# Performance work log

Hardware: AMD Instinct MI355X
Metric: run time of the kernel (lower is better)

## Reference

```python
import jax, jax.numpy as jnp
import numpy as np

B, S, D = 8, 1024, 2048
H, HD = 16, 128          # n_heads, head_dim (H*HD == D)
ROPE = 64                # rotary dims per head (front slice)
MAXB, MAXS = 10, 1024    # kv-cache buffer sizes (hardcoded in module)
START_POS = 0


def _apply_rope(x, cos_half, sin_half):
    # x: (BH, S, ROPE); cos/sin_half: (S, ROPE//2) -> tiled to (S, ROPE)
    cos_full = jnp.concatenate([cos_half, cos_half], axis=-1)
    sin_full = jnp.concatenate([sin_half, sin_half], axis=-1)
    half = x.shape[-1] // 2
    x1, x2 = x[..., :half], x[..., half:]
    rotated = jnp.concatenate([-x2, x1], axis=-1)
    return x * cos_full + rotated * sin_full


def setup_inputs() -> dict:
    key = jax.random.key(0)
    ks = jax.random.split(key, 6)
    sc = 0.02
    x = jax.random.normal(ks[0], (B, S, D), dtype=jnp.float32)
    wq = jax.random.normal(ks[1], (D, D), dtype=jnp.float32) * sc
    wk = jax.random.normal(ks[2], (D, D), dtype=jnp.float32) * sc
    wv = jax.random.normal(ks[3], (D, D), dtype=jnp.float32) * sc
    wo = jax.random.normal(ks[4], (D, D), dtype=jnp.float32) * sc
    bq = jnp.zeros((D,), jnp.float32)
    bk = jnp.zeros((D,), jnp.float32)
    bv = jnp.zeros((D,), jnp.float32)
    bo = jnp.zeros((D,), jnp.float32)
    # RoPE tables (HF "half" layout): angles over positions
    half = ROPE // 2
    inv_freq = 1.0 / (10000.0 ** (jnp.arange(half, dtype=jnp.float32) / half))
    ang = jnp.arange(S, dtype=jnp.float32)[:, None] * inv_freq[None, :]  # (S, half)
    cos_half = jnp.cos(ang)
    sin_half = jnp.sin(ang)
    mask = jnp.zeros((S, S), jnp.float32)  # additive mask, (seq, end_pos)
    cache_k = jnp.zeros((MAXB, MAXS, H * HD), jnp.float32)
    cache_v = jnp.zeros((MAXB, MAXS, H * HD), jnp.float32)
    return {
        "x": x, "wq": wq, "bq": bq, "wk": wk, "bk": bk, "wv": wv, "bv": bv,
        "wo": wo, "bo": bo, "cos_half": cos_half, "sin_half": sin_half,
        "mask": mask, "cache_k": cache_k, "cache_v": cache_v,
        "start_pos": START_POS,
    }


def reference(x, wq, bq, wk, bk, wv, bv, wo, bo, cos_half, sin_half, mask,
              cache_k, cache_v, start_pos):
    b, s, _ = x.shape
    end_pos = start_pos + s
    # QKV projections (torch Linear: y = x @ W.T + b)
    q = (x @ wq.T + bq).reshape(b, s, H, HD)
    k = (x @ wk.T + bk).reshape(b, s, H, HD)
    v = (x @ wv.T + bv).reshape(b, s, H, HD)
    # Partial RoPE on the first ROPE dims of each head
    q_head = q[..., :ROPE].transpose(0, 2, 1, 3).reshape(b * H, s, ROPE)
    k_head = k[..., :ROPE].transpose(0, 2, 1, 3).reshape(b * H, s, ROPE)
    q_head = _apply_rope(q_head, cos_half, sin_half)
    k_head = _apply_rope(k_head, cos_half, sin_half)
    q_head = q_head.reshape(b, H, s, ROPE).transpose(0, 2, 1, 3)
    k_head = k_head.reshape(b, H, s, ROPE).transpose(0, 2, 1, 3)
    q = jnp.concatenate([q_head, q[..., ROPE:]], axis=-1)
    k = jnp.concatenate([k_head, k[..., ROPE:]], axis=-1)
    # KV-cache write then read (start_pos is a static python int)
    cache_k = jax.lax.dynamic_update_slice(cache_k, k.reshape(b, s, H * HD), (0, start_pos, 0))
    cache_v = jax.lax.dynamic_update_slice(cache_v, v.reshape(b, s, H * HD), (0, start_pos, 0))
    k_cached = cache_k[:b, :end_pos].reshape(b, end_pos, H, HD)
    v_cached = cache_v[:b, :end_pos].reshape(b, end_pos, H, HD)
    # Unnormalized attention: no softmax, no scaling
    scores = jnp.einsum('bshd,bthd->bsht', q, k_cached)  # (B,S,H,T)
    scores = scores + mask[:, None, :]                   # (S,1,T) broadcast
    a_sum = jnp.einsum('bsht,bthd->bshd', scores, v_cached)
    out = a_sum.reshape(b, s, H * HD) @ wo.T + bo
    return out
```

## Files before the change

kernel.cpp:

```cpp
#include <hip/hip_runtime.h>
#include <stdint.h>

#define B_ 8
#define S_ 1024
#define D_ 2048
#define H_ 16
#define HD_ 128
#define NROW 8192
#define NQKV 6144

typedef __bf16 bf16;
typedef bf16  bf16x8 __attribute__((ext_vector_type(8)));
typedef bf16  bf16x4 __attribute__((ext_vector_type(4)));
typedef float f32x4  __attribute__((ext_vector_type(4)));

#define AS1 __attribute__((address_space(1)))
#define AS3 __attribute__((address_space(3)))

__device__ __forceinline__ void gl_lds16(const bf16* g, bf16* l) {
  __builtin_amdgcn_global_load_lds((AS1 void*)g, (AS3 void*)l, 16, 0, 0);
}

__global__ __launch_bounds__(256) void prep(const float* __restrict__ x,
                                            const float* __restrict__ wq,
                                            const float* __restrict__ wk,
                                            const float* __restrict__ wv,
                                            const float* __restrict__ wo,
                                            const float* __restrict__ mask,
                                            const float* __restrict__ bq,
                                            const float* __restrict__ bk,
                                            const float* __restrict__ bv,
                                            bf16* __restrict__ xb,
                                            bf16* __restrict__ wqkvb,
                                            bf16* __restrict__ wob,
                                            bf16* __restrict__ maskb,
                                            float* __restrict__ bqkv) {
  long i = (long)blockIdx.x * 256 + threadIdx.x;
  if (i < 8650752) {
    const float* src; bf16* dst; long j;
    if (i < 4194304)      { src = x;    dst = xb;              j = i; }
    else if (i < 5242880) { src = wq;   dst = wqkvb;           j = i - 4194304; }
    else if (i < 6291456) { src = wk;   dst = wqkvb + 4194304; j = i - 5242880; }
    else if (i < 7340032) { src = wv;   dst = wqkvb + 8388608; j = i - 6291456; }
    else if (i < 8388608) { src = wo;   dst = wob;             j = i - 7340032; }
    else                  { src = mask; dst = maskb;           j = i - 8388608; }
    float4 v = reinterpret_cast<const float4*>(src)[j];
    bf16x4 o;
    o.x = (bf16)v.x; o.y = (bf16)v.y; o.z = (bf16)v.z; o.w = (bf16)v.w;
    reinterpret_cast<bf16x4*>(dst)[j] = o;
  } else {
    long e = (i - 8650752) * 4;
    const float* s = (e < 2048) ? bq + e : (e < 4096 ? bk + (e - 2048) : bv + (e - 4096));
    *reinterpret_cast<float4*>(bqkv + e) = *reinterpret_cast<const float4*>(s);
  }
}

#define READ_A4(QA, KS, Ab)                                                   \
  _Pragma("unroll") for (int mi = 0; mi < 4; mi++)                            \
    af[mi] = *reinterpret_cast<const bf16x8*>(                                \
        (Ab) + aoff + ((((QA)*4 + mi)*2) + (KS))*512);

#define READ_B4(KS, Bb)                                                       \
  _Pragma("unroll") for (int ni = 0; ni < 4; ni++)                            \
    bfr[ni] = *reinterpret_cast<const bf16x8*>(                               \
        (Bb) + boff + ((ni*2) + (KS))*512);

#define MFMA16(QA)                                                            \
  _Pragma("unroll") for (int mi = 0; mi < 4; mi++)                            \
  _Pragma("unroll") for (int ni = 0; ni < 4; ni++)                            \
    acc[(QA)*4 + mi][ni] = __builtin_amdgcn_mfma_f32_16x16x32_bf16(           \
        af[mi], bfr[ni], acc[(QA)*4 + mi][ni], 0, 0, 0);

#define STAGE_H0(An, Bn, koff)                                                \
  gl_lds16(agA + (koff),           (An) + wid*1024);                          \
  gl_lds16(agA + 128*la + (koff),  (An) + (wid + 8)*1024);                    \
  gl_lds16(agB + (koff),           (Bn) + wid*1024);                          \
  gl_lds16(agB + 128*lb + (koff),  (Bn) + (wid + 8)*1024);

#define STAGE_H1(An, Bn, koff)                                                \
  gl_lds16(agA + (koff) + 32,          (An) + wid*1024 + 512);                \
  gl_lds16(agA + 128*la + (koff) + 32, (An) + (wid + 8)*1024 + 512);          \
  gl_lds16(agB + (koff) + 32,          (Bn) + wid*1024 + 512);                \
  gl_lds16(agB + 128*lb + (koff) + 32, (Bn) + (wid + 8)*1024 + 512);

template <typename CT, bool BIAS, bool ACCUM>
__global__ __launch_bounds__(512, 2) void gemm256(const bf16* __restrict__ A,
                                                  const bf16* __restrict__ Bm,
                                                  const float* __restrict__ bias,
                                                  CT* __restrict__ C,
                                                  int M, int N, int K,
                                                  long la, long lb, long lc,
                                                  long za, long zb, long zc) {
  extern __shared__ __align__(16) bf16 lds[];
  const int z = blockIdx.z;
  A  += (long)z * za;
  Bm += (long)z * zb;
  C  += (long)z * zc;
  const int tid  = threadIdx.x;
  const int wid  = tid >> 6;
  const int lane = tid & 63;
  const int wm0 = (wid >> 2) * 128;
  const int wn0 = (wid & 3) * 64;
  const int m0 = blockIdx.y * 256, n0 = blockIdx.x * 256;

  const int rr = lane >> 2;
  const int cc = ((lane & 3) * 8) ^ ((rr & 8) << 1);
  const bf16* agA = A  + (long)(m0 + wid * 16 + rr) * la + cc;
  const bf16* agB = Bm + (long)(n0 + wid * 16 + rr) * lb + cc;

  const int swz  = ((lane >> 4) * 8) ^ ((lane & 8) << 1);
  const int aoff = (wm0 >> 4) * 1024 + (lane & 15) * 32 + swz;
  const int boff = (wn0 >> 4) * 1024 + (lane & 15) * 32 + swz;

  f32x4 acc[8][4] = {};
  const int NT = K >> 6;

  { bf16* An = lds; bf16* Bn = lds + 16384;
    STAGE_H0(An, Bn, 0); STAGE_H1(An, Bn, 0); }
  { bf16* An = lds + 32768; bf16* Bn = lds + 49152;
    STAGE_H0(An, Bn, 64); }

  for (int t = 0; t < NT; ++t) {
    const bf16* Ab = lds + (t & 1) * 32768;
    const bf16* Bb = Ab + 16384;
    bf16* An1 = lds + ((t & 1) ^ 1) * 32768;
    bf16* Bn1 = An1 + 16384;
    bf16* An2 = lds + (t & 1) * 32768;
    bf16* Bn2 = An2 + 16384;
    const bool pf1 = (t + 1) < NT;
    const bool pf2 = (t + 2) < NT;
    bf16x8 af[4], bfr[4];

    if (pf1) asm volatile("s_waitcnt vmcnt(8)" ::: "memory");
    else     asm volatile("s_waitcnt vmcnt(4)" ::: "memory");
    __builtin_amdgcn_s_barrier();
    READ_A4(0, 0, Ab); READ_B4(0, Bb);
    if (pf1) { STAGE_H1(An1, Bn1, (long)(t + 1) * 64); }
    asm volatile("s_waitcnt lgkmcnt(0)" ::: "memory");
    __builtin_amdgcn_sched_barrier(0);
    __builtin_amdgcn_s_setprio(1); MFMA16(0); __builtin_amdgcn_s_setprio(0);

    READ_A4(1, 0, Ab);
    asm volatile("s_waitcnt lgkmcnt(0)" ::: "memory");
    __builtin_amdgcn_sched_barrier(0);
    __builtin_amdgcn_s_setprio(1); MFMA16(1); __builtin_amdgcn_s_setprio(0);

    if (pf1) asm volatile("s_waitcnt vmcnt(8)" ::: "memory");
    else     asm volatile("s_waitcnt vmcnt(0)" ::: "memory");
    __builtin_amdgcn_s_barrier();
    READ_A4(0, 1, Ab); READ_B4(1, Bb);
    if (pf2) { STAGE_H0(An2, Bn2, (long)(t + 2) * 64); }
    asm volatile("s_waitcnt lgkmcnt(0)" ::: "memory");
    __builtin_amdgcn_sched_barrier(0);
    __builtin_amdgcn_s_setprio(1); MFMA16(0); __builtin_amdgcn_s_setprio(0);

    READ_A4(1, 1, Ab);
    asm volatile("s_waitcnt lgkmcnt(0)" ::: "memory");
    __builtin_amdgcn_sched_barrier(0);
    __builtin_amdgcn_s_setprio(1); MFMA16(1); __builtin_amdgcn_s_setprio(0);
  }

#pragma unroll
  for (int mi = 0; mi < 8; mi++) {
#pragma unroll
    for (int ni = 0; ni < 4; ni++) {
      const int col = n0 + wn0 + ni * 16 + (lane & 15);
      float bv = 0.0f;
      if constexpr (BIAS) bv = bias[col];
      const long base = (long)(m0 + wm0 + mi * 16 + (lane >> 4) * 4) * lc + col;
#pragma unroll
      for (int r = 0; r < 4; r++) {
        float v = acc[mi][ni][r] + bv;
        if constexpr (ACCUM) v += (float)C[base + (long)r * lc];
        C[base + (long)r * lc] = (CT)v;
      }
    }
  }
}

template <typename CT, bool BIAS, bool ACCUM>
__global__ __launch_bounds__(256) void gemm_bt(const bf16* __restrict__ A,
                                               const bf16* __restrict__ Bm,
                                               const float* __restrict__ bias,
                                               CT* __restrict__ C,
                                               int M, int N, int K,
                                               long la, long lb, long lc,
                                               long za, long zb, long zc) {
  __shared__ __align__(16) bf16 As[128 * 32];
  __shared__ __align__(16) bf16 Bs[128 * 32];
  const int z = blockIdx.z;
  A  += (long)z * za;
  Bm += (long)z * zb;
  C  += (long)z * zc;
  const int tid = threadIdx.x;
  const int w = tid >> 6, l = tid & 63;
  const int wm = (w & 1) * 64, wn = (w >> 1) * 64;
  const int m0 = blockIdx.y * 128, n0 = blockIdx.x * 128;
  const int lr = l & 15, lk = (l >> 4) * 8;
  const int er = (l >> 4) * 4;

  const bf16* ag = A  + (long)(m0 + (tid >> 2)) * la + (tid & 3) * 8;
  const bf16* bg = Bm + (long)(n0 + (tid >> 2)) * lb + (tid & 3) * 8;
  bf16* al = As + (w * 16) * 32;
  bf16* bl = Bs + (w * 16) * 32;

  f32x4 acc[4][4] = {};

  for (int k0 = 0; k0 < K; k0 += 32) {
    gl_lds16(ag + k0,            al);
    gl_lds16(ag + 64 * la + k0,  al + 64 * 32);
    gl_lds16(bg + k0,            bl);
    gl_lds16(bg + 64 * lb + k0,  bl + 64 * 32);
    __syncthreads();
    bf16x8 afr[4], bfr[4];
#pragma unroll
    for (int mi = 0; mi < 4; mi++)
      afr[mi] = *reinterpret_cast<const bf16x8*>(As + (wm + mi * 16 + lr) * 32 + lk);
#pragma unroll
    for (int ni = 0; ni < 4; ni++)
      bfr[ni] = *reinterpret_cast<const bf16x8*>(Bs + (wn + ni * 16 + lr) * 32 + lk);
#pragma unroll
    for (int mi = 0; mi < 4; mi++)
#pragma unroll
      for (int ni = 0; ni < 4; ni++)
        acc[mi][ni] = __builtin_amdgcn_mfma_f32_16x16x32_bf16(afr[mi], bfr[ni], acc[mi][ni], 0, 0, 0);
    __syncthreads();
  }

#pragma unroll
  for (int mi = 0; mi < 4; mi++) {
#pragma unroll
    for (int ni = 0; ni < 4; ni++) {
      const int col = n0 + wn + ni * 16 + lr;
      float bv = 0.0f;
      if constexpr (BIAS) bv = bias[col];
      const long base = (long)(m0 + wm + mi * 16 + er) * lc + col;
#pragma unroll
      for (int r = 0; r < 4; r++) {
        float v = acc[mi][ni][r] + bv;
        if constexpr (ACCUM) v += (float)C[base + (long)r * lc];
        C[base + (long)r * lc] = (CT)v;
      }
    }
  }
}

__global__ __launch_bounds__(256) void rope_qk(bf16* __restrict__ QKV,
                                               const float* __restrict__ ch,
                                               const float* __restrict__ sh) {
  int idx = blockIdx.x * 256 + threadIdx.x;
  if (idx >= NROW * H_ * 2 * 32) return;
  int hd = idx & 31;
  int qk = (idx >> 5) & 1;
  int h  = (idx >> 6) & 15;
  int row = idx >> 10;
  int s = row & (S_ - 1);
  long base = (long)row * NQKV + qk * 2048 + h * HD_ + hd;
  float a  = (float)QKV[base];
  float b2 = (float)QKV[base + 32];
  float c = ch[s * 32 + hd], sn = sh[s * 32 + hd];
  QKV[base]      = (bf16)(a * c - b2 * sn);
  QKV[base + 32] = (bf16)(b2 * c + a * sn);
}

__global__ __launch_bounds__(256) void kvtrans(const bf16* __restrict__ QKV,
                                               bf16* __restrict__ Kt,
                                               bf16* __restrict__ Vt) {
  __shared__ unsigned short T[128 * 130];
  const int bid = blockIdx.x;
  const int tb = bid & 7, bh = (bid >> 3) & 127, kv = bid >> 10;
  const int b = bh >> 4, h = bh & 15;
  const int tid = threadIdx.x;
  const bf16* src = QKV + (long)(b * S_ + tb * 128) * NQKV + 2048 + kv * 2048 + h * HD_;
#pragma unroll
  for (int it = 0; it < 8; it++) {
    int chunk = it * 256 + tid;
    int r = chunk >> 4, hc = (chunk & 15) * 8;
    bf16x8 v = *reinterpret_cast<const bf16x8*>(src + (long)r * NQKV + hc);
    union { bf16x8 v8; unsigned short u[8]; } u8; u8.v8 = v;
#pragma unroll
    for (int j = 0; j < 8; j++) T[r * 130 + hc + j] = u8.u[j];
  }
  __syncthreads();
  bf16* dst = (kv ? Vt : Kt) + (long)bh * HD_ * S_ + tb * 128;
#pragma unroll
  for (int it = 0; it < 8; it++) {
    int chunk = it * 256 + tid;
    int hd = chunk >> 4, tc = (chunk & 15) * 8;
    union { bf16x8 v8; unsigned short u[8]; } u8;
#pragma unroll
    for (int j = 0; j < 8; j++) u8.u[j] = T[(tc + j) * 130 + hd];
    *reinterpret_cast<bf16x8*>(dst + (long)hd * S_ + tc) = u8.v8;
  }
}

__global__ __launch_bounds__(256) void qw2_gemm(const bf16* __restrict__ QKV,
                                                const bf16* __restrict__ W2,
                                                bf16* __restrict__ Ob) {
  __shared__ __align__(16) bf16 As[128 * 32];
  __shared__ __align__(16) bf16 Bs[128 * 32];
  const int z = blockIdx.z;
  const int b = z >> 4, h = z & 15;
  const int m0 = blockIdx.y * 128;
  const int tid = threadIdx.x;
  const int w = tid >> 6, l = tid & 63;
  const int wm = (w & 1) * 64, wn = (w >> 1) * 64;
  const int lr = l & 15, lk = (l >> 4) * 8;
  const int er = (l >> 4) * 4;

  const bf16* ag = QKV + (long)(b * S_ + m0 + (tid >> 2)) * NQKV + h * HD_ + (tid & 3) * 8;
  const bf16* bg = W2 + (long)z * (HD_ * HD_) + (tid >> 2) * HD_ + (tid & 3) * 8;
  bf16* al = As + (w * 16) * 32;
  bf16* bl = Bs + (w * 16) * 32;

  f32x4 acc[4][4] = {};

#pragma unroll
  for (int k0 = 0; k0 < HD_; k0 += 32) {
    gl_lds16(ag + k0,                   al);
    gl_lds16(ag + (long)64 * NQKV + k0, al + 64 * 32);
    gl_lds16(bg + k0,                   bl);
    gl_lds16(bg + 64 * HD_ + k0,        bl + 64 * 32);
    __syncthreads();
    bf16x8 afr[4], bfr[4];
#pragma unroll
    for (int mi = 0; mi < 4; mi++)
      afr[mi] = *reinterpret_cast<const bf16x8*>(As + (wm + mi * 16 + lr) * 32 + lk);
#pragma unroll
    for (int ni = 0; ni < 4; ni++)
      bfr[ni] = *reinterpret_cast<const bf16x8*>(Bs + (wn + ni * 16 + lr) * 32 + lk);
#pragma unroll
    for (int mi = 0; mi < 4; mi++)
#pragma unroll
      for (int ni = 0; ni < 4; ni++)
        acc[mi][ni] = __builtin_amdgcn_mfma_f32_16x16x32_bf16(afr[mi], bfr[ni], acc[mi][ni], 0, 0, 0);
    __syncthreads();
  }

#pragma unroll
  for (int mi = 0; mi < 4; mi++) {
#pragma unroll
    for (int ni = 0; ni < 4; ni++) {
      const int col = h * HD_ + wn + ni * 16 + lr;
#pragma unroll
      for (int r = 0; r < 4; r++) {
        const int sl = m0 + wm + mi * 16 + er + r;
        const long idx = (long)(b * S_ + sl) * D_ + col;
        Ob[idx] = (bf16)((float)Ob[idx] + acc[mi][ni][r]);
      }
    }
  }
}

extern "C" void kernel_launch(void* const* d_in, const int* in_sizes, int n_in,
                              void* d_out, int out_size, void* d_ws, size_t ws_size,
                              hipStream_t stream) {
  const float* x   = (const float*)d_in[0];
  const float* wq  = (const float*)d_in[1];
  const float* bq  = (const float*)d_in[2];
  const float* wk  = (const float*)d_in[3];
  const float* bk  = (const float*)d_in[4];
  const float* wv  = (const float*)d_in[5];
  const float* bv  = (const float*)d_in[6];
  const float* wo  = (const float*)d_in[7];
  const float* bo  = (const float*)d_in[8];
  const float* ch  = (const float*)d_in[9];
  const float* sh  = (const float*)d_in[10];
  const float* mask = (const float*)d_in[11];
  float* out = (float*)d_out;

  hipFuncSetAttribute(reinterpret_cast<const void*>(&gemm256<bf16, true, false>),
                      hipFuncAttributeMaxDynamicSharedMemorySize, 131072);
  hipFuncSetAttribute(reinterpret_cast<const void*>(&gemm256<bf16, false, false>),
                      hipFuncAttributeMaxDynamicSharedMemorySize, 131072);
  hipFuncSetAttribute(reinterpret_cast<const void*>(&gemm256<float, true, false>),
                      hipFuncAttributeMaxDynamicSharedMemorySize, 131072);

  char* ws = (char*)d_ws;
  bf16*  QKV   = (bf16*)(ws);
  bf16*  Vt    = (bf16*)(ws + 100663296);
  bf16*  Kt    = (bf16*)(ws + 134217728);
  bf16*  wob   = (bf16*)(ws + 167772160);
  float* bqkv  = (float*)(ws + 176160768);
  bf16*  maskb = (bf16*)(ws + 176185344);
  bf16*  W2    = (bf16*)(ws + 178282496);
  bf16*  Ob    = (bf16*)(ws + 182476800);
  bf16*  xb    = (bf16*)(ws + 216031232);
  bf16*  wqkvb = (bf16*)(ws + 249585664);

  prep<<<33798, 256, 0, stream>>>(x, wq, wk, wv, wo, mask, bq, bk, bv,
                                  xb, wqkvb, wob, maskb, bqkv);

  gemm256<bf16, true, false><<<dim3(24, 32, 1), 512, 131072, stream>>>(
      xb, wqkvb, bqkv, QKV, NROW, NQKV, D_,
      (long)D_, (long)D_, (long)NQKV, 0L, 0L, 0L);

  rope_qk<<<32768, 256, 0, stream>>>(QKV, ch, sh);
  kvtrans<<<2048, 256, 0, stream>>>(QKV, Kt, Vt);

  gemm_bt<bf16, false, false><<<dim3(1, 1, 128), 256, 0, stream>>>(
      Vt, Kt, nullptr, W2, HD_, HD_, S_,
      (long)S_, (long)S_, (long)HD_,
      (long)(HD_ * S_), (long)(HD_ * S_), (long)(HD_ * HD_));

  gemm256<bf16, false, false><<<dim3(8, 4, 8), 512, 131072, stream>>>(
      maskb, Vt, nullptr, Ob, S_, D_, S_,
      (long)S_, (long)S_, (long)D_,
      0L, (long)(D_ * S_), (long)(S_ * D_));

  qw2_gemm<<<dim3(1, 8, 128), 256, 0, stream>>>(QKV, W2, Ob);

  gemm256<float, true, false><<<dim3(8, 32, 1), 512, 131072, stream>>>(
      Ob, wob, bo, out, NROW, D_, D_,
      (long)D_, (long)D_, (long)D_, 0L, 0L, 0L);
}
```

Before: 630.3 us.

## Fuse RoPE into QKV GEMM epilogue and merge mask-V with Q·W2 GEMM

After: 605.2 us. 1.04x faster.

```diff
diff --git a/kernel.cpp b/kernel.cpp
--- a/kernel.cpp
+++ b/kernel.cpp
@@ -83,14 +83,52 @@
   gl_lds16(agB + (koff) + 32,          (Bn) + wid*1024 + 512);                \
   gl_lds16(agB + 128*lb + (koff) + 32, (Bn) + (wid + 8)*1024 + 512);
 
-template <typename CT, bool BIAS, bool ACCUM>
+#define GEMM256_MAIN_LOOP(NT)                                                 \
+  { bf16* An = lds; bf16* Bn = lds + 16384;                                   \
+    STAGE_H0(An, Bn, 0); STAGE_H1(An, Bn, 0); }                               \
+  for (int t = 0; t < (NT); ++t) {                                            \
+    const bf16* Ab = lds + (t & 1) * 32768;                                   \
+    const bf16* Bb = Ab + 16384;                                              \
+    bf16* An = lds + ((t & 1) ^ 1) * 32768;                                   \
+    bf16* Bn = An + 16384;                                                    \
+    const long kn = (long)(t + 1) * 64;                                       \
+    const bool pf = (t + 1) < (NT);                                           \
+    bf16x8 af[4], bfr[4];                                                     \
+    asm volatile("s_waitcnt vmcnt(4)" ::: "memory");                          \
+    __builtin_amdgcn_s_barrier();                                             \
+    READ_A4(0, 0, Ab); READ_B4(0, Bb);                                        \
+    if (pf) { STAGE_H0(An, Bn, kn); }                                         \
+    asm volatile("s_waitcnt lgkmcnt(0)" ::: "memory");                        \
+    __builtin_amdgcn_sched_barrier(0);                                        \
+    __builtin_amdgcn_s_setprio(1); MFMA16(0); __builtin_amdgcn_s_setprio(0);  \
+    READ_A4(1, 0, Ab);                                                        \
+    asm volatile("s_waitcnt lgkmcnt(0)" ::: "memory");                        \
+    __builtin_amdgcn_sched_barrier(0);                                        \
+    __builtin_amdgcn_s_setprio(1); MFMA16(1); __builtin_amdgcn_s_setprio(0);  \
+    if (pf) asm volatile("s_waitcnt vmcnt(4)" ::: "memory");                  \
+    else    asm volatile("s_waitcnt vmcnt(0)" ::: "memory");                  \
+    __builtin_amdgcn_s_barrier();                                             \
+    READ_A4(0, 1, Ab); READ_B4(1, Bb);                                        \
+    if (pf) { STAGE_H1(An, Bn, kn); }                                         \
+    asm volatile("s_waitcnt lgkmcnt(0)" ::: "memory");                        \
+    __builtin_amdgcn_sched_barrier(0);                                        \
+    __builtin_amdgcn_s_setprio(1); MFMA16(0); __builtin_amdgcn_s_setprio(0);  \
+    READ_A4(1, 1, Ab);                                                        \
+    asm volatile("s_waitcnt lgkmcnt(0)" ::: "memory");                        \
+    __builtin_amdgcn_sched_barrier(0);                                        \
+    __builtin_amdgcn_s_setprio(1); MFMA16(1); __builtin_amdgcn_s_setprio(0);  \
+  }
+
+template <typename CT, bool BIAS, bool ACCUM, bool ROPE>
 __global__ __launch_bounds__(512, 2) void gemm256(const bf16* __restrict__ A,
                                                   const bf16* __restrict__ Bm,
                                                   const float* __restrict__ bias,
                                                   CT* __restrict__ C,
                                                   int M, int N, int K,
                                                   long la, long lb, long lc,
-                                                  long za, long zb, long zc) {
+                                                  long za, long zb, long zc,
+                                                  const float* __restrict__ chp,
+                                                  const float* __restrict__ shp) {
   extern __shared__ __align__(16) bf16 lds[];
   const int z = blockIdx.z;
   A  += (long)z * za;
@@ -115,65 +153,150 @@
   f32x4 acc[8][4] = {};
   const int NT = K >> 6;
 
-  { bf16* An = lds; bf16* Bn = lds + 16384;
-    STAGE_H0(An, Bn, 0); STAGE_H1(An, Bn, 0); }
-  { bf16* An = lds + 32768; bf16* Bn = lds + 49152;
-    STAGE_H0(An, Bn, 64); }
-
-  for (int t = 0; t < NT; ++t) {
-    const bf16* Ab = lds + (t & 1) * 32768;
-    const bf16* Bb = Ab + 16384;
-    bf16* An1 = lds + ((t & 1) ^ 1) * 32768;
-    bf16* Bn1 = An1 + 16384;
-    bf16* An2 = lds + (t & 1) * 32768;
-    bf16* Bn2 = An2 + 16384;
-    const bool pf1 = (t + 1) < NT;
-    const bool pf2 = (t + 2) < NT;
-    bf16x8 af[4], bfr[4];
-
-    if (pf1) asm volatile("s_waitcnt vmcnt(8)" ::: "memory");
-    else     asm volatile("s_waitcnt vmcnt(4)" ::: "memory");
-    __builtin_amdgcn_s_barrier();
-    READ_A4(0, 0, Ab); READ_B4(0, Bb);
-    if (pf1) { STAGE_H1(An1, Bn1, (long)(t + 1) * 64); }
-    asm volatile("s_waitcnt lgkmcnt(0)" ::: "memory");
-    __builtin_amdgcn_sched_barrier(0);
-    __builtin_amdgcn_s_setprio(1); MFMA16(0); __builtin_amdgcn_s_setprio(0);
-
-    READ_A4(1, 0, Ab);
-    asm volatile("s_waitcnt lgkmcnt(0)" ::: "memory");
-    __builtin_amdgcn_sched_barrier(0);
-    __builtin_amdgcn_s_setprio(1); MFMA16(1); __builtin_amdgcn_s_setprio(0);
-
-    if (pf1) asm volatile("s_waitcnt vmcnt(8)" ::: "memory");
-    else     asm volatile("s_waitcnt vmcnt(0)" ::: "memory");
-    __builtin_amdgcn_s_barrier();
-    READ_A4(0, 1, Ab); READ_B4(1, Bb);
-    if (pf2) { STAGE_H0(An2, Bn2, (long)(t + 2) * 64); }
-    asm volatile("s_waitcnt lgkmcnt(0)" ::: "memory");
-    __builtin_amdgcn_sched_barrier(0);
-    __builtin_amdgcn_s_setprio(1); MFMA16(0); __builtin_amdgcn_s_setprio(0);
-
-    READ_A4(1, 1, Ab);
-    asm volatile("s_waitcnt lgkmcnt(0)" ::: "memory");
-    __builtin_amdgcn_sched_barrier(0);
-    __builtin_amdgcn_s_setprio(1); MFMA16(1); __builtin_amdgcn_s_setprio(0);
-  }
+  GEMM256_MAIN_LOOP(NT);
 
 #pragma unroll
   for (int mi = 0; mi < 8; mi++) {
+    float vals[4][4];
 #pragma unroll
     for (int ni = 0; ni < 4; ni++) {
       const int col = n0 + wn0 + ni * 16 + (lane & 15);
       float bv = 0.0f;
       if constexpr (BIAS) bv = bias[col];
+#pragma unroll
+      for (int r = 0; r < 4; r++) vals[ni][r] = acc[mi][ni][r] + bv;
+    }
+    if constexpr (ROPE) {
+      if ((n0 + wn0) < 4096 && (((n0 + wn0) & 127) == 0)) {
+#pragma unroll
+        for (int ni = 0; ni < 2; ni++)
+#pragma unroll
+          for (int r = 0; r < 4; r++) {
+            const int srow = (m0 + wm0 + mi * 16 + (lane >> 4) * 4 + r) & (S_ - 1);
+            const int hd = ni * 16 + (lane & 15);
+            const float c  = chp[srow * 32 + hd];
+            const float sn = shp[srow * 32 + hd];
+            const float a  = vals[ni][r], b2 = vals[ni + 2][r];
+            vals[ni][r]     = a * c - b2 * sn;
+            vals[ni + 2][r] = b2 * c + a * sn;
+          }
+      }
+    }
+#pragma unroll
+    for (int ni = 0; ni < 4; ni++) {
+      const int col = n0 + wn0 + ni * 16 + (lane & 15);
       const long base = (long)(m0 + wm0 + mi * 16 + (lane >> 4) * 4) * lc + col;
 #pragma unroll
       for (int r = 0; r < 4; r++) {
-        float v = acc[mi][ni][r] + bv;
+        float v = vals[ni][r];
         if constexpr (ACCUM) v += (float)C[base + (long)r * lc];
         C[base + (long)r * lc] = (CT)v;
       }
+    }
+  }
+}
+
+__global__ __launch_bounds__(512, 2) void pv256(const bf16* __restrict__ Am,
+                                                const bf16* __restrict__ Vt,
+                                                const bf16* __restrict__ QKV,
+                                                const bf16* __restrict__ W2,
+                                                bf16* __restrict__ Ob) {
+  extern __shared__ __align__(16) bf16 lds[];
+  const int z = blockIdx.z;
+  const bf16* A  = Am;
+  const bf16* Bm = Vt + (long)z * (D_ * S_);
+  bf16* C = Ob + (long)z * (S_ * D_);
+  const long la = S_, lb = S_;
+  const int tid  = threadIdx.x;
+  const int wid  = tid >> 6;
+  const int lane = tid & 63;
+  const int wm0 = (wid >> 2) * 128;
+  const int wn0 = (wid & 3) * 64;
+  const int m0 = blockIdx.y * 256, n0 = blockIdx.x * 256;
+
+  const int rr = lane >> 2;
+  const int cc = ((lane & 3) * 8) ^ ((rr & 8) << 1);
+  const bf16* agA = A  + (long)(m0 + wid * 16 + rr) * la + cc;
+  const bf16* agB = Bm + (long)(n0 + wid * 16 + rr) * lb + cc;
+
+  const int swz  = ((lane >> 4) * 8) ^ ((lane & 8) << 1);
+  const int aoff = (wm0 >> 4) * 1024 + (lane & 15) * 32 + swz;
+  const int boff = (wn0 >> 4) * 1024 + (lane & 15) * 32 + swz;
+
+  f32x4 acc[8][4] = {};
+
+  GEMM256_MAIN_LOOP(16);
+
+  const int h0 = n0 >> 7;
+  const int hsel = wn0 >> 7;
+  const int a2base = hsel * 16384;
+  const int b2base = 32768 + hsel * 8192;
+  const int bsub = (wn0 & 64) >> 4;
+  const int a2off = (wm0 >> 4) * 1024 + (lane & 15) * 32 + swz;
+  const int b2off = (lane & 15) * 32 + swz;
+
+#define STAGE_K2(e0)                                                          \
+  { const bf16* qa0 = QKV + (long)(z * S_ + m0 + wid * 16 + rr) * NQKV        \
+                      + h0 * 128 + (e0) + cc;                                 \
+    gl_lds16(qa0,                       lds + wid * 1024);                    \
+    gl_lds16(qa0 + 32,                  lds + wid * 1024 + 512);              \
+    gl_lds16(qa0 + 128 * NQKV,          lds + (wid + 8) * 1024);              \
+    gl_lds16(qa0 + 128 * NQKV + 32,     lds + (wid + 8) * 1024 + 512);        \
+    gl_lds16(qa0 + 128,                 lds + 16384 + wid * 1024);            \
+    gl_lds16(qa0 + 160,                 lds + 16384 + wid * 1024 + 512);      \
+    gl_lds16(qa0 + 128 * NQKV + 128,    lds + 16384 + (wid + 8) * 1024);      \
+    gl_lds16(qa0 + 128 * NQKV + 160,    lds + 16384 + (wid + 8) * 1024 + 512);\
+    const bf16* w0 = W2 + (long)(z * 16 + h0) * 16384                         \
+                     + (wid * 16 + rr) * 128 + (e0) + cc;                     \
+    gl_lds16(w0,                        lds + 32768 + wid * 1024);            \
+    gl_lds16(w0 + 32,                   lds + 32768 + wid * 1024 + 512);      \
+    gl_lds16(w0 + 16384,                lds + 40960 + wid * 1024);            \
+    gl_lds16(w0 + 16384 + 32,           lds + 40960 + wid * 1024 + 512);      }
+
+  __builtin_amdgcn_s_barrier();
+  STAGE_K2(0);
+#pragma unroll
+  for (int step = 0; step < 2; step++) {
+    asm volatile("s_waitcnt vmcnt(0)" ::: "memory");
+    __builtin_amdgcn_s_barrier();
+    bf16x8 a2[8], b2[4];
+#pragma unroll
+    for (int ks = 0; ks < 2; ks++) {
+#pragma unroll
+      for (int mi = 0; mi < 8; mi++)
+        a2[mi] = *reinterpret_cast<const bf16x8*>(
+            lds + a2base + a2off + mi * 1024 + ks * 512);
+#pragma unroll
+      for (int ni = 0; ni < 4; ni++)
+        b2[ni] = *reinterpret_cast<const bf16x8*>(
+            lds + b2base + b2off + (bsub + ni) * 1024 + ks * 512);
+      asm volatile("s_waitcnt lgkmcnt(0)" ::: "memory");
+      __builtin_amdgcn_sched_barrier(0);
+      __builtin_amdgcn_s_setprio(1);
+#pragma unroll
+      for (int mi = 0; mi < 8; mi++)
+#pragma unroll
+        for (int ni = 0; ni < 4; ni++)
+          acc[mi][ni] = __builtin_amdgcn_mfma_f32_16x16x32_bf16(
+              a2[mi], b2[ni], acc[mi][ni], 0, 0, 0);
+      __builtin_amdgcn_s_setprio(0);
+    }
+    if (step == 0) {
+      __builtin_amdgcn_s_barrier();
+      STAGE_K2(64);
+    }
+  }
+#undef STAGE_K2
+
+#pragma unroll
+  for (int mi = 0; mi < 8; mi++) {
+#pragma unroll
+    for (int ni = 0; ni < 4; ni++) {
+      const int col = n0 + wn0 + ni * 16 + (lane & 15);
+      const long base = (long)(m0 + wm0 + mi * 16 + (lane >> 4) * 4) * D_ + col;
+#pragma unroll
+      for (int r = 0; r < 4; r++)
+        C[base + (long)r * D_] = (bf16)acc[mi][ni][r];
     }
   }
 }
@@ -245,24 +368,6 @@
   }
 }
 
-__global__ __launch_bounds__(256) void rope_qk(bf16* __restrict__ QKV,
-                                               const float* __restrict__ ch,
-                                               const float* __restrict__ sh) {
-  int idx = blockIdx.x * 256 + threadIdx.x;
-  if (idx >= NROW * H_ * 2 * 32) return;
-  int hd = idx & 31;
-  int qk = (idx >> 5) & 1;
-  int h  = (idx >> 6) & 15;
-  int row = idx >> 10;
-  int s = row & (S_ - 1);
-  long base = (long)row * NQKV + qk * 2048 + h * HD_ + hd;
-  float a  = (float)QKV[base];
-  float b2 = (float)QKV[base + 32];
-  float c = ch[s * 32 + hd], sn = sh[s * 32 + hd];
-  QKV[base]      = (bf16)(a * c - b2 * sn);
-  QKV[base + 32] = (bf16)(b2 * c + a * sn);
-}
-
 __global__ __launch_bounds__(256) void kvtrans(const bf16* __restrict__ QKV,
                                                bf16* __restrict__ Kt,
                                                bf16* __restrict__ Vt) {
@@ -291,64 +396,6 @@
 #pragma unroll
     for (int j = 0; j < 8; j++) u8.u[j] = T[(tc + j) * 130 + hd];
     *reinterpret_cast<bf16x8*>(dst + (long)hd * S_ + tc) = u8.v8;
-  }
-}
-
-__global__ __launch_bounds__(256) void qw2_gemm(const bf16* __restrict__ QKV,
-                                                const bf16* __restrict__ W2,
-                                                bf16* __restrict__ Ob) {
-  __shared__ __align__(16) bf16 As[128 * 32];
-  __shared__ __align__(16) bf16 Bs[128 * 32];
-  const int z = blockIdx.z;
-  const int b = z >> 4, h = z & 15;
-  const int m0 = blockIdx.y * 128;
-  const int tid = threadIdx.x;
-  const int w = tid >> 6, l = tid & 63;
-  const int wm = (w & 1) * 64, wn = (w >> 1) * 64;
-  const int lr = l & 15, lk = (l >> 4) * 8;
-  const int er = (l >> 4) * 4;
-
-  const bf16* ag = QKV + (long)(b * S_ + m0 + (tid >> 2)) * NQKV + h * HD_ + (tid & 3) * 8;
-  const bf16* bg = W2 + (long)z * (HD_ * HD_) + (tid >> 2) * HD_ + (tid & 3) * 8;
-  bf16* al = As + (w * 16) * 32;
-  bf16* bl = Bs + (w * 16) * 32;
-
-  f32x4 acc[4][4] = {};
-
-#pragma unroll
-  for (int k0 = 0; k0 < HD_; k0 += 32) {
-    gl_lds16(ag + k0,                   al);
-    gl_lds16(ag + (long)64 * NQKV + k0, al + 64 * 32);
-    gl_lds16(bg + k0,                   bl);
-    gl_lds16(bg + 64 * HD_ + k0,        bl + 64 * 32);
-    __syncthreads();
-    bf16x8 afr[4], bfr[4];
-#pragma unroll
-    for (int mi = 0; mi < 4; mi++)
-      afr[mi] = *reinterpret_cast<const bf16x8*>(As + (wm + mi * 16 + lr) * 32 + lk);
-#pragma unroll
-    for (int ni = 0; ni < 4; ni++)
-      bfr[ni] = *reinterpret_cast<const bf16x8*>(Bs + (wn + ni * 16 + lr) * 32 + lk);
-#pragma unroll
-    for (int mi = 0; mi < 4; mi++)
-#pragma unroll
-      for (int ni = 0; ni < 4; ni++)
-        acc[mi][ni] = __builtin_amdgcn_mfma_f32_16x16x32_bf16(afr[mi], bfr[ni], acc[mi][ni], 0, 0, 0);
-    __syncthreads();
-  }
-
-#pragma unroll
-  for (int mi = 0; mi < 4; mi++) {
-#pragma unroll
-    for (int ni = 0; ni < 4; ni++) {
-      const int col = h * HD_ + wn + ni * 16 + lr;
-#pragma unroll
-      for (int r = 0; r < 4; r++) {
-        const int sl = m0 + wm + mi * 16 + er + r;
-        const long idx = (long)(b * S_ + sl) * D_ + col;
-        Ob[idx] = (bf16)((float)Ob[idx] + acc[mi][ni][r]);
-      }
-    }
   }
 }
 
@@ -369,11 +416,11 @@
   const float* mask = (const float*)d_in[11];
   float* out = (float*)d_out;
 
-  hipFuncSetAttribute(reinterpret_cast<const void*>(&gemm256<bf16, true, false>),
+  hipFuncSetAttribute(reinterpret_cast<const void*>(&gemm256<bf16, true, false, true>),
                       hipFuncAttributeMaxDynamicSharedMemorySize, 131072);
-  hipFuncSetAttribute(reinterpret_cast<const void*>(&gemm256<bf16, false, false>),
+  hipFuncSetAttribute(reinterpret_cast<const void*>(&gemm256<float, true, false, false>),
                       hipFuncAttributeMaxDynamicSharedMemorySize, 131072);
-  hipFuncSetAttribute(reinterpret_cast<const void*>(&gemm256<float, true, false>),
+  hipFuncSetAttribute(reinterpret_cast<const void*>(&pv256),
                       hipFuncAttributeMaxDynamicSharedMemorySize, 131072);
 
   char* ws = (char*)d_ws;
@@ -391,11 +438,10 @@
   prep<<<33798, 256, 0, stream>>>(x, wq, wk, wv, wo, mask, bq, bk, bv,
                                   xb, wqkvb, wob, maskb, bqkv);
 
-  gemm256<bf16, true, false><<<dim3(24, 32, 1), 512, 131072, stream>>>(
+  gemm256<bf16, true, false, true><<<dim3(24, 32, 1), 512, 131072, stream>>>(
       xb, wqkvb, bqkv, QKV, NROW, NQKV, D_,
-      (long)D_, (long)D_, (long)NQKV, 0L, 0L, 0L);
-
-  rope_qk<<<32768, 256, 0, stream>>>(QKV, ch, sh);
+      (long)D_, (long)D_, (long)NQKV, 0L, 0L, 0L, ch, sh);
+
   kvtrans<<<2048, 256, 0, stream>>>(QKV, Kt, Vt);
 
   gemm_bt<bf16, false, false><<<dim3(1, 1, 128), 256, 0, stream>>>(
@@ -403,14 +449,9 @@
       (long)S_, (long)S_, (long)HD_,
       (long)(HD_ * S_), (long)(HD_ * S_), (long)(HD_ * HD_));
 
-  gemm256<bf16, false, false><<<dim3(8, 4, 8), 512, 131072, stream>>>(
-      maskb, Vt, nullptr, Ob, S_, D_, S_,
-      (long)S_, (long)S_, (long)D_,
-      0L, (long)(D_ * S_), (long)(S_ * D_));
-
-  qw2_gemm<<<dim3(1, 8, 128), 256, 0, stream>>>(QKV, W2, Ob);
-
-  gemm256<float, true, false><<<dim3(8, 32, 1), 512, 131072, stream>>>(
+  pv256<<<dim3(8, 4, 8), 512, 131072, stream>>>(maskb, Vt, QKV, W2, Ob);
+
+  gemm256<float, true, false, false><<<dim3(8, 32, 1), 512, 131072, stream>>>(
       Ob, wob, bo, out, NROW, D_, D_,
-      (long)D_, (long)D_, (long)D_, 0L, 0L, 0L);
-}
+      (long)D_, (long)D_, (long)D_, 0L, 0L, 0L, nullptr, nullptr);
+}
```
